# Performance work log

Measured on AMD Instinct MI355X. Metric: run time of the kernel, lower is better.

Reference implementation:

```python
import jax, jax.numpy as jnp
import numpy as np

D_X, D_H, N_I = 1024, 64, 16  # model dim, per-head dim (d_q=d_k=d_v), heads
BSZ, SEQ = 2, 2048


def _linear(x, W, b):
    return x @ W.T + b


def setup_inputs() -> dict:
    key = jax.random.key(0)
    ks = jax.random.split(key, 16)
    s_in = 1.0 / np.sqrt(D_X)
    s_hd = 1.0 / np.sqrt(N_I * D_H)
    return {
        "query": jax.random.normal(ks[0], (BSZ, SEQ, D_X), jnp.float32),
        "key": jax.random.normal(ks[1], (BSZ, SEQ, D_X), jnp.float32),
        "value": jax.random.normal(ks[2], (BSZ, SEQ, D_X), jnp.float32),
        "Wq": jax.random.normal(ks[3], (N_I * D_H, D_X), jnp.float32) * s_in,
        "bq": jnp.zeros((N_I * D_H,), jnp.float32),
        "Wk": jax.random.normal(ks[4], (N_I * D_H, D_X), jnp.float32) * s_in,
        "bk": jnp.zeros((N_I * D_H,), jnp.float32),
        "Wv": jax.random.normal(ks[5], (N_I * D_H, D_X), jnp.float32) * s_in,
        "bv": jnp.zeros((N_I * D_H,), jnp.float32),
        "Wxv": jax.random.normal(ks[6], (N_I * D_H, D_X), jnp.float32) * s_in,
        "bxv": jnp.zeros((N_I * D_H,), jnp.float32),
        "Wxo": jax.random.normal(ks[7], (D_X, N_I * D_H), jnp.float32) * s_hd,
        "bxo": jnp.zeros((D_X,), jnp.float32),
        "Wmo": jax.random.normal(ks[8], (D_X, N_I * D_H), jnp.float32) * s_hd,
        "bmo": jnp.zeros((D_X,), jnp.float32),
    }


def reference(query, key, value, Wq, bq, Wk, bk, Wv, bv, Wxv, bxv, Wxo, bxo, Wmo, bmo):
    bsz, seq, _ = query.shape

    def heads(x):  # (b, s, n_I*d) -> (b, h, s, d)
        return x.reshape(bsz, seq, N_I, D_H).transpose(0, 2, 1, 3)

    Q = heads(_linear(query, Wq, bq))
    K = heads(_linear(key, Wk, bk))
    V = heads(_linear(value, Wv, bv))

    dot = jnp.einsum('bhid,bhjd->bhij', Q, K) / jnp.sqrt(jnp.float32(D_H))
    attention = jax.nn.softmax(dot, axis=-1)  # dropout p=0 (eval)

    # use_xv=True: replace K with xV = W_xv(key) for the k_bar aggregation
    xV = heads(_linear(key, Wxv, bxv))

    k_bar = jnp.einsum('bhjd,bhij->bhid', xV, attention)
    v_bar = jnp.einsum('bhjd,bhij->bhid', V, attention)

    def merge(x):  # (b, h, s, d) -> (b, s, h*d)
        return x.transpose(0, 2, 1, 3).reshape(bsz, seq, N_I * D_H)

    x = _linear(merge(k_bar), Wxo, bxo)
    m = _linear(merge(v_bar), Wmo, bmo)
    return (x, m)
```

## Files before the change

kernel.cpp:

```cpp
#include <hip/hip_runtime.h>
#include <math.h>

typedef __bf16 bf16;
typedef __bf16 bf16x2 __attribute__((ext_vector_type(2)));
typedef __bf16 bf16x4 __attribute__((ext_vector_type(4)));
typedef __bf16 bf16x8 __attribute__((ext_vector_type(8)));
typedef float f32x4 __attribute__((ext_vector_type(4)));

#define SEQ 2048
#define DH 64
#define DX 1024
#define NH 16
#define LP 72

static __device__ __forceinline__ f32x4 mfma16(bf16x8 a, bf16x8 b, f32x4 c) {
    return __builtin_amdgcn_mfma_f32_16x16x32_bf16(a, b, c, 0, 0, 0);
}
static __device__ __forceinline__ bf16x8 cvt8(const float* __restrict__ p) {
    f32x4 a = *(const f32x4*)p;
    f32x4 b = *(const f32x4*)(p + 4);
    bf16x8 r;
    #pragma unroll
    for (int j = 0; j < 4; ++j) { r[j] = (bf16)a[j]; r[4 + j] = (bf16)b[j]; }
    return r;
}

#define GL16(gp, lp) __builtin_amdgcn_global_load_lds( \
    (const __attribute__((address_space(1))) void*)(gp), \
    (__attribute__((address_space(3))) void*)(lp), 16, 0, 0)


__global__ __launch_bounds__(256) void cvt_all(
    const float* __restrict__ q, const float* __restrict__ k,
    const float* __restrict__ v,
    const float* __restrict__ w0, const float* __restrict__ w1,
    const float* __restrict__ w2, const float* __restrict__ w3,
    const float* __restrict__ w4, const float* __restrict__ w5,
    bf16* __restrict__ out)
{
    const size_t i = (size_t)blockIdx.x * 2048 + threadIdx.x * 8;
    const int seg = (int)(i >> 20);
    const float* s;
    size_t off;
    if (seg < 4)       { s = q; off = i; }
    else if (seg < 8)  { s = k; off = i - (4ull << 20); }
    else if (seg < 12) { s = v; off = i - (8ull << 20); }
    else {
        const float* ww[6] = {w0, w1, w2, w3, w4, w5};
        s = ww[seg - 12]; off = i - ((size_t)seg << 20);
    }
    *(bf16x8*)(out + i) = cvt8(s + off);
}

struct G4 {
    const bf16* X[4]; const bf16* W[4]; const float* B[4];
    bf16* Yb[4]; float* Yf[4]; int xmode[4]; int ymode[4];
};

template<int BM>
__global__ __launch_bounds__(512) void gemm256(G4 a)
{
    constexpr int MREP = BM / 32;
    __shared__ __align__(16) bf16 As[2][BM * 64];
    __shared__ __align__(16) bf16 Bs[2][256 * 64];

    const int z = blockIdx.z;
    const bf16* __restrict__ X = a.X[z];
    const bf16* __restrict__ W = a.W[z];
    const int xmode = a.xmode[z], ymode = a.ymode[z];

    const int tid  = threadIdx.x;
    const int wid  = tid >> 6;
    const int lane = tid & 63;
    const int l16  = lane & 15;
    const int quad = lane >> 4;
    const int wm   = wid >> 2;
    const int wn   = wid & 3;
    const int m0 = blockIdx.y * BM;
    const int n0 = blockIdx.x * 256;

    const int srow8 = lane >> 3;
    const int sch   = (lane & 7) ^ srow8;

    f32x4 acc[MREP][4];
    #pragma unroll
    for (int i = 0; i < MREP; ++i)
        #pragma unroll
        for (int j = 0; j < 4; ++j) acc[i][j] = (f32x4){0.f,0.f,0.f,0.f};

    auto stage = [&](int buf, int kb) {
        #pragma unroll
        for (int g = 0; g < BM / 64; ++g) {
            const int row = g * 64 + wid * 8 + srow8;
            const bf16* src;
            if (xmode == 0) {
                src = X + (size_t)(m0 + row) * DX + kb * 64 + sch * 8;
            } else {
                const int m = m0 + row;
                const int b = m >> 11, s = m & 2047;
                src = X + ((size_t)(b * NH + kb) * SEQ + s) * DH + sch * 8;
            }
            GL16(src, &As[buf][(g * 64 + wid * 8) * 64]);
        }
        #pragma unroll
        for (int g = 0; g < 4; ++g) {
            const int row = g * 64 + wid * 8 + srow8;
            const bf16* src = W + (size_t)(n0 + row) * DX + kb * 64 + sch * 8;
            GL16(src, &Bs[buf][(g * 64 + wid * 8) * 64]);
        }
    };

    stage(0, 0);
    __syncthreads();

    int cur = 0;
    for (int kb = 0; kb < DX / 64; ++kb) {
        if (kb + 1 < DX / 64) stage(cur ^ 1, kb + 1);
        #pragma unroll
        for (int ks = 0; ks < 2; ++ks) {
            bf16x8 af[MREP], bfr[4];
            const int cc = (ks * 4 + quad) ^ (l16 & 7);
            #pragma unroll
            for (int mf = 0; mf < MREP; ++mf)
                af[mf] = *(const bf16x8*)&As[cur][(wm * (BM/2) + mf * 16 + l16) * 64 + cc * 8];
            #pragma unroll
            for (int nf = 0; nf < 4; ++nf)
                bfr[nf] = *(const bf16x8*)&Bs[cur][(wn * 64 + nf * 16 + l16) * 64 + cc * 8];
            #pragma unroll
            for (int mf = 0; mf < MREP; ++mf)
                #pragma unroll
                for (int nf = 0; nf < 4; ++nf)
                    acc[mf][nf] = mfma16(af[mf], bfr[nf], acc[mf][nf]);
        }
        __syncthreads();
        cur ^= 1;
    }

    #pragma unroll
    for (int nf = 0; nf < 4; ++nf) {
        const int col = n0 + wn * 64 + nf * 16 + l16;
        const float bvv = a.B[z][col];
        #pragma unroll
        for (int mf = 0; mf < MREP; ++mf) {
            #pragma unroll
            for (int r = 0; r < 4; ++r) {
                const int row = m0 + wm * (BM/2) + mf * 16 + quad * 4 + r;
                const float vv = acc[mf][nf][r] + bvv;
                if (ymode == 0) {
                    const int b = row >> 11, s = row & 2047;
                    const int h = col >> 6, d = col & 63;
                    a.Yb[z][((size_t)(b * NH + h) * SEQ + s) * DH + d] = (bf16)vv;
                } else {
                    a.Yf[z][(size_t)row * DX + col] = vv;
                }
            }
        }
    }
}

__global__ __launch_bounds__(256) void attn_fast(
    bf16* __restrict__ Q, const bf16* __restrict__ K,
    const bf16* __restrict__ V, const bf16* __restrict__ xV,
    bf16* __restrict__ VB)
{
    __shared__ __align__(16) bf16 Ks[2][64 * 64];
    __shared__ __align__(16) bf16 Vt [64 * LP];
    __shared__ __align__(16) bf16 xVt[64 * LP];
    __shared__ __align__(16) bf16 Pl[4][32 * LP];

    const int tid  = threadIdx.x;
    const int wave = tid >> 6;
    const int lane = tid & 63;
    const int l16  = lane & 15;
    const int quad = lane >> 4;
    const size_t hb = ((size_t)blockIdx.z * NH + blockIdx.y) * SEQ * DH;
    const int q0 = blockIdx.x * 128 + wave * 32;

    bf16x8 qf[2][2];
    #pragma unroll
    for (int mf = 0; mf < 2; ++mf)
        #pragma unroll
        for (int ks = 0; ks < 2; ++ks)
            qf[mf][ks] = *(const bf16x8*)(Q + hb + (size_t)(q0 + mf*16 + l16) * DH + ks*32 + quad*8);

    bf16x8 one8;
    #pragma unroll
    for (int j = 0; j < 8; ++j) one8[j] = (bf16)1.0f;

    f32x4 ov[2][4], oxv[2][4];
    f32x4 rsa[2];
    rsa[0] = (f32x4){0.f,0.f,0.f,0.f};
    rsa[1] = (f32x4){0.f,0.f,0.f,0.f};
    #pragma unroll
    for (int mf = 0; mf < 2; ++mf)
        #pragma unroll
        for (int c = 0; c < 4; ++c) {
            ov[mf][c]  = (f32x4){0.f,0.f,0.f,0.f};
            oxv[mf][c] = (f32x4){0.f,0.f,0.f,0.f};
        }

    const int krow = lane >> 3;
    const int kch  = (lane & 7) ^ krow;
    const int vkp = (tid & 31) * 2;
    const int vd0 = (tid >> 5) * 8;
    const float SCL = 0.125f * 1.4426950408889634f;

    bf16x8 pv0, pv1, px0, px1;
    {
        const bf16* kg = K + hb + (size_t)(wave*16 + krow) * DH + kch*8;
        GL16(kg,            &Ks[0][(wave*16 + 0) * 64]);
        GL16(kg + 8 * DH,   &Ks[0][(wave*16 + 8) * 64]);
        const size_t g0 = hb + (size_t)vkp * DH + vd0;
        pv0 = *(const bf16x8*)(V  + g0);
        pv1 = *(const bf16x8*)(V  + g0 + DH);
        px0 = *(const bf16x8*)(xV + g0);
        px1 = *(const bf16x8*)(xV + g0 + DH);
    }

    int c = 0;
    for (int kt = 0; kt < SEQ; kt += 64) {
        #pragma unroll
        for (int j = 0; j < 8; ++j) {
            *(bf16x2*)&Vt [(vd0 + j) * LP + vkp] = (bf16x2){pv0[j], pv1[j]};
            *(bf16x2*)&xVt[(vd0 + j) * LP + vkp] = (bf16x2){px0[j], px1[j]};
        }
        if (kt + 64 < SEQ) {
            const bf16* kg = K + hb + (size_t)(kt + 64 + wave*16 + krow) * DH + kch*8;
            GL16(kg,          &Ks[c ^ 1][(wave*16 + 0) * 64]);
            GL16(kg + 8 * DH, &Ks[c ^ 1][(wave*16 + 8) * 64]);
            const size_t g0 = hb + (size_t)(kt + 64 + vkp) * DH + vd0;
            pv0 = *(const bf16x8*)(V  + g0);
            pv1 = *(const bf16x8*)(V  + g0 + DH);
            px0 = *(const bf16x8*)(xV + g0);
            px1 = *(const bf16x8*)(xV + g0 + DH);
        }
        __asm__ volatile("s_waitcnt lgkmcnt(0)" ::: "memory");
        __builtin_amdgcn_s_barrier();
        __asm__ volatile("s_waitcnt vmcnt(6)" ::: "memory");
        __builtin_amdgcn_sched_barrier(0);

        f32x4 sf[4][2];
        #pragma unroll
        for (int mf = 0; mf < 4; ++mf)
            #pragma unroll
            for (int nf = 0; nf < 2; ++nf) sf[mf][nf] = (f32x4){0.f,0.f,0.f,0.f};
        __builtin_amdgcn_s_setprio(1);
        #pragma unroll
        for (int ks = 0; ks < 2; ++ks)
            #pragma unroll
            for (int mf = 0; mf < 4; ++mf) {
                bf16x8 kf = *(const bf16x8*)&Ks[c][(mf*16 + l16) * 64 +
                                                   (((ks*4 + quad) ^ (l16 & 7)) * 8)];
                sf[mf][0] = mfma16(kf, qf[0][ks], sf[mf][0]);
                sf[mf][1] = mfma16(kf, qf[1][ks], sf[mf][1]);
            }
        __builtin_amdgcn_s_setprio(0);

        #pragma unroll
        for (int nf = 0; nf < 2; ++nf)
            #pragma unroll
            for (int mf = 0; mf < 4; ++mf) {
                float p0 = __builtin_amdgcn_exp2f(sf[mf][nf][0] * SCL);
                float p1 = __builtin_amdgcn_exp2f(sf[mf][nf][1] * SCL);
                float p2 = __builtin_amdgcn_exp2f(sf[mf][nf][2] * SCL);
                float p3 = __builtin_amdgcn_exp2f(sf[mf][nf][3] * SCL);
                *(bf16x4*)&Pl[wave][(nf * 16 + l16) * LP + mf * 16 + quad * 4] =
                    (bf16x4){(bf16)p0, (bf16)p1, (bf16)p2, (bf16)p3};
            }
        __asm__ volatile("s_waitcnt lgkmcnt(0)" ::: "memory");
        __builtin_amdgcn_sched_barrier(0);

        __builtin_amdgcn_s_setprio(1);
        #pragma unroll
        for (int ks = 0; ks < 2; ++ks) {
            bf16x8 pa0 = *(const bf16x8*)&Pl[wave][(l16)      * LP + ks * 32 + quad * 8];
            bf16x8 pa1 = *(const bf16x8*)&Pl[wave][(16 + l16) * LP + ks * 32 + quad * 8];
            rsa[0] = mfma16(pa0, one8, rsa[0]);
            rsa[1] = mfma16(pa1, one8, rsa[1]);
            #pragma unroll
            for (int cc = 0; cc < 4; ++cc) {
                bf16x8 bv = *(const bf16x8*)&Vt [(cc * 16 + l16) * LP + ks * 32 + quad * 8];
                ov[0][cc]  = mfma16(pa0, bv, ov[0][cc]);
                ov[1][cc]  = mfma16(pa1, bv, ov[1][cc]);
                bf16x8 bx = *(const bf16x8*)&xVt[(cc * 16 + l16) * LP + ks * 32 + quad * 8];
                oxv[0][cc] = mfma16(pa0, bx, oxv[0][cc]);
                oxv[1][cc] = mfma16(pa1, bx, oxv[1][cc]);
            }
        }
        __builtin_amdgcn_s_setprio(0);

        __builtin_amdgcn_sched_barrier(0);
        __builtin_amdgcn_s_barrier();
        c ^= 1;
    }

    #pragma unroll
    for (int mf = 0; mf < 2; ++mf)
        #pragma unroll
        for (int r = 0; r < 4; ++r) {
            const int qrow = mf * 16 + quad * 4 + r;
            const float inv = 1.0f / rsa[mf][r];
            const size_t base = hb + (size_t)(q0 + qrow) * DH;
            #pragma unroll
            for (int cc = 0; cc < 4; ++cc) {
                const int d = cc * 16 + l16;
                Q [base + d] = (bf16)(oxv[mf][cc][r] * inv);
                VB[base + d] = (bf16)(ov[mf][cc][r]  * inv);
            }
        }
}


__global__ __launch_bounds__(256) void proj_gemm(
    const void* __restrict__ Xv, const float* __restrict__ W,
    const float* __restrict__ bias, void* __restrict__ Yv,
    int in_kind, int out_mode)
{
    __shared__ __align__(16) bf16 As[64 * LP];
    __shared__ __align__(16) bf16 Bs[128 * LP];
    const int tid  = threadIdx.x;
    const int wave = tid >> 6;
    const int lane = tid & 63;
    const int l16  = lane & 15;
    const int quad = lane >> 4;
    const int m0 = blockIdx.y * 64;
    const int n0 = blockIdx.x * 128;
    const int m_w = (wave >> 1) * 32;
    const int n_w = (wave & 1) * 64;
    const int ar = tid >> 2, ac = (tid & 3) * 16;
    const int br = tid >> 1, bc = (tid & 1) * 32;

    f32x4 acc[2][4];
    #pragma unroll
    for (int i = 0; i < 2; ++i)
        #pragma unroll
        for (int j = 0; j < 4; ++j) acc[i][j] = (f32x4){0.f,0.f,0.f,0.f};

    for (int kb = 0; kb < DX / 64; ++kb) {
        __syncthreads();
        if (in_kind == 0) {
            const float* xp = (const float*)Xv + (size_t)(m0 + ar) * DX + kb * 64 + ac;
            *(bf16x8*)&As[ar * LP + ac]     = cvt8(xp);
            *(bf16x8*)&As[ar * LP + ac + 8] = cvt8(xp + 8);
        } else {
            const bf16* xp = (const bf16*)Xv + ((size_t)kb * SEQ + (m0 + ar)) * DH + ac;
            *(bf16x8*)&As[ar * LP + ac]     = *(const bf16x8*)xp;
            *(bf16x8*)&As[ar * LP + ac + 8] = *(const bf16x8*)(xp + 8);
        }
        {
            const float* wp = W + (size_t)(n0 + br) * DX + kb * 64 + bc;
            #pragma unroll
            for (int g = 0; g < 4; ++g)
                *(bf16x8*)&Bs[br * LP + bc + g * 8] = cvt8(wp + g * 8);
        }
        __syncthreads();
        #pragma unroll
        for (int ks = 0; ks < 2; ++ks) {
            bf16x8 a0 = *(const bf16x8*)&As[(m_w + l16)      * LP + ks * 32 + quad * 8];
            bf16x8 a1 = *(const bf16x8*)&As[(m_w + 16 + l16) * LP + ks * 32 + quad * 8];
            #pragma unroll
            for (int nf = 0; nf < 4; ++nf) {
                bf16x8 b = *(const bf16x8*)&Bs[(n_w + nf * 16 + l16) * LP + ks * 32 + quad * 8];
                acc[0][nf] = mfma16(a0, b, acc[0][nf]);
                acc[1][nf] = mfma16(a1, b, acc[1][nf]);
            }
        }
    }
    #pragma unroll
    for (int mf = 0; mf < 2; ++mf)
        #pragma unroll
        for (int nf = 0; nf < 4; ++nf) {
            const int col = n0 + n_w + nf * 16 + l16;
            const float bvv = bias[col];
            #pragma unroll
            for (int r = 0; r < 4; ++r) {
                const int row = m0 + m_w + mf * 16 + quad * 4 + r;
                float v = acc[mf][nf][r] + bvv;
                if (out_mode == 0) {
                    int h = col >> 6, d = col & 63;
                    ((bf16*)Yv)[((size_t)h * SEQ + row) * DH + d] = (bf16)v;
                } else {
                    ((float*)Yv)[(size_t)row * DX + col] = v;
                }
            }
        }
}

__global__ __launch_bounds__(256) void attn_dual(
    bf16* __restrict__ Q, const bf16* __restrict__ K,
    const bf16* __restrict__ V, const bf16* __restrict__ xV,
    bf16* __restrict__ vb)
{
    __shared__ __align__(16) bf16 Ks [64 * LP];
    __shared__ __align__(16) bf16 Vt [64 * LP];
    __shared__ __align__(16) bf16 xVt[64 * LP];
    __shared__ __align__(16) bf16 Pl[4][32 * LP];
    const int tid  = threadIdx.x;
    const int h    = blockIdx.y;
    const int qt   = blockIdx.x;
    const int wave = tid >> 6;
    const int lane = tid & 63;
    const int l16  = lane & 15;
    const int quad = lane >> 4;
    const size_t hb = (size_t)h * SEQ * DH;
    const int q0 = qt * 128 + wave * 32;

    bf16x8 qf[2][2];
    #pragma unroll
    for (int mf = 0; mf < 2; ++mf)
        #pragma unroll
        for (int ks = 0; ks < 2; ++ks)
            qf[mf][ks] = *(const bf16x8*)(Q + hb + (size_t)(q0 + mf*16 + l16) * DH + ks*32 + quad*8);

    float mr[2][4], lr[2][4];
    f32x4 ov[2][4], oxv[2][4];
    #pragma unroll
    for (int mf = 0; mf < 2; ++mf)
        #pragma unroll
        for (int r = 0; r < 4; ++r) { mr[mf][r] = -1e30f; lr[mf][r] = 0.f; }
    #pragma unroll
    for (int mf = 0; mf < 2; ++mf)
        #pragma unroll
        for (int c = 0; c < 4; ++c) {
            ov[mf][c]  = (f32x4){0.f,0.f,0.f,0.f};
            oxv[mf][c] = (f32x4){0.f,0.f,0.f,0.f};
        }
    const int sr = tid >> 2, sc = (tid & 3) * 16;
    const int vkp = (tid & 31) * 2;
    const int vd0 = (tid >> 5) * 8;
    const float SCL = 0.125f * 1.4426950408889634f;

    for (int kt = 0; kt < SEQ; kt += 64) {
        __syncthreads();
        {
            const bf16* kpt = K + hb + (size_t)(kt + sr) * DH + sc;
            *(bf16x8*)&Ks[sr * LP + sc]     = *(const bf16x8*)kpt;
            *(bf16x8*)&Ks[sr * LP + sc + 8] = *(const bf16x8*)(kpt + 8);
            const size_t g0 = hb + (size_t)(kt + vkp) * DH + vd0;
            bf16x8 v0 = *(const bf16x8*)(V + g0);
            bf16x8 v1 = *(const bf16x8*)(V + g0 + DH);
            bf16x8 x0 = *(const bf16x8*)(xV + g0);
            bf16x8 x1 = *(const bf16x8*)(xV + g0 + DH);
            #pragma unroll
            for (int j = 0; j < 8; ++j) {
                *(bf16x2*)&Vt [(vd0 + j) * LP + vkp] = (bf16x2){v0[j], v1[j]};
                *(bf16x2*)&xVt[(vd0 + j) * LP + vkp] = (bf16x2){x0[j], x1[j]};
            }
        }
        __syncthreads();
        f32x4 sf[2][4];
        #pragma unroll
        for (int mf = 0; mf < 2; ++mf)
            #pragma unroll
            for (int nf = 0; nf < 4; ++nf) sf[mf][nf] = (f32x4){0.f,0.f,0.f,0.f};
        #pragma unroll
        for (int ks = 0; ks < 2; ++ks)
            #pragma unroll
            for (int nf = 0; nf < 4; ++nf) {
                bf16x8 bk = *(const bf16x8*)&Ks[(nf * 16 + l16) * LP + ks * 32 + quad * 8];
                sf[0][nf] = mfma16(qf[0][ks], bk, sf[0][nf]);
                sf[1][nf] = mfma16(qf[1][ks], bk, sf[1][nf]);
            }
        float mx[2][4], rs[2][4], alpha[2][4];
        #pragma unroll
        for (int mf = 0; mf < 2; ++mf)
            #pragma unroll
            for (int r = 0; r < 4; ++r) {
                float aa = fmaxf(sf[mf][0][r], sf[mf][1][r]);
                float bb = fmaxf(sf[mf][2][r], sf[mf][3][r]);
                mx[mf][r] = fmaxf(aa, bb) * SCL;
            }
        #pragma unroll
        for (int off = 1; off < 16; off <<= 1)
            #pragma unroll
            for (int mf = 0; mf < 2; ++mf)
                #pragma unroll
                for (int r = 0; r < 4; ++r)
                    mx[mf][r] = fmaxf(mx[mf][r], __shfl_xor(mx[mf][r], off, 64));
        #pragma unroll
        for (int mf = 0; mf < 2; ++mf)
            #pragma unroll
            for (int r = 0; r < 4; ++r) {
                float mnew = fmaxf(mr[mf][r], mx[mf][r]);
                alpha[mf][r] = exp2f(mr[mf][r] - mnew);
                mr[mf][r] = mnew;
            }
        bf16* pw = &Pl[wave][0];
        #pragma unroll
        for (int mf = 0; mf < 2; ++mf)
            #pragma unroll
            for (int r = 0; r < 4; ++r) rs[mf][r] = 0.f;
        #pragma unroll
        for (int mf = 0; mf < 2; ++mf)
            #pragma unroll
            for (int nf = 0; nf < 4; ++nf)
                #pragma unroll
                for (int r = 0; r < 4; ++r) {
                    float p = exp2f(sf[mf][nf][r] * SCL - mr[mf][r]);
                    rs[mf][r] += p;
                    pw[(mf * 16 + quad * 4 + r) * LP + nf * 16 + l16] = (bf16)p;
                }
        #pragma unroll
        for (int off = 1; off < 16; off <<= 1)
            #pragma unroll
            for (int mf = 0; mf < 2; ++mf)
                #pragma unroll
                for (int r = 0; r < 4; ++r)
                    rs[mf][r] += __shfl_xor(rs[mf][r], off, 64);
        #pragma unroll
        for (int mf = 0; mf < 2; ++mf)
            #pragma unroll
            for (int r = 0; r < 4; ++r)
                lr[mf][r] = lr[mf][r] * alpha[mf][r] + rs[mf][r];
        #pragma unroll
        for (int mf = 0; mf < 2; ++mf)
            #pragma unroll
            for (int c = 0; c < 4; ++c)
                #pragma unroll
                for (int r = 0; r < 4; ++r) {
                    ov[mf][c][r]  *= alpha[mf][r];
                    oxv[mf][c][r] *= alpha[mf][r];
                }
        __asm__ volatile("s_waitcnt lgkmcnt(0)" ::: "memory");
        #pragma unroll
        for (int ks = 0; ks < 2; ++ks) {
            bf16x8 pa0 = *(const bf16x8*)&Pl[wave][(l16)      * LP + ks * 32 + quad * 8];
            bf16x8 pa1 = *(const bf16x8*)&Pl[wave][(16 + l16) * LP + ks * 32 + quad * 8];
            #pragma unroll
            for (int c = 0; c < 4; ++c) {
                bf16x8 bv = *(const bf16x8*)&Vt [(c * 16 + l16) * LP + ks * 32 + quad * 8];
                ov[0][c]  = mfma16(pa0, bv, ov[0][c]);
                ov[1][c]  = mfma16(pa1, bv, ov[1][c]);
                bf16x8 bx = *(const bf16x8*)&xVt[(c * 16 + l16) * LP + ks * 32 + quad * 8];
                oxv[0][c] = mfma16(pa0, bx, oxv[0][c]);
                oxv[1][c] = mfma16(pa1, bx, oxv[1][c]);
            }
        }
    }
    #pragma unroll
    for (int mf = 0; mf < 2; ++mf)
        #pragma unroll
        for (int r = 0; r < 4; ++r) {
            const int s = q0 + mf * 16 + quad * 4 + r;
            const float inv = 1.0f / lr[mf][r];
            #pragma unroll
            for (int c = 0; c < 4; ++c) {
                const int d = c * 16 + l16;
                Q [hb + (size_t)s * DH + d] = (bf16)(oxv[mf][c][r] * inv);
                vb[hb + (size_t)s * DH + d] = (bf16)(ov[mf][c][r]  * inv);
            }
        }
}


extern "C" void kernel_launch(void* const* d_in, const int* in_sizes, int n_in,
                              void* d_out, int out_size, void* d_ws, size_t ws_size,
                              hipStream_t stream) {
    const float* query = (const float*)d_in[0];
    const float* key   = (const float*)d_in[1];
    const float* value = (const float*)d_in[2];
    const float* Wq  = (const float*)d_in[3];  const float* bq  = (const float*)d_in[4];
    const float* Wk  = (const float*)d_in[5];  const float* bk  = (const float*)d_in[6];
    const float* Wv  = (const float*)d_in[7];  const float* bv  = (const float*)d_in[8];
    const float* Wxv = (const float*)d_in[9];  const float* bxv = (const float*)d_in[10];
    const float* Wxo = (const float*)d_in[11]; const float* bxo = (const float*)d_in[12];
    const float* Wmo = (const float*)d_in[13]; const float* bmo = (const float*)d_in[14];

    float* out = (float*)d_out;
    const size_t SB = (size_t)SEQ * DX;
    const size_t M1 = 1ull << 20;

    dim3 blk(256);

    if (ws_size >= (76ull << 20)) {
        bf16* ws = (bf16*)d_ws;
        bf16* qb  = ws;
        bf16* kb  = ws + 4 * M1;
        bf16* vb  = ws + 8 * M1;
        bf16* Wqb = ws + 12 * M1;
        bf16* Wkb = Wqb + M1;
        bf16* Wvb = Wkb + M1;
        bf16* Wxvb= Wvb + M1;
        bf16* Wxob= Wxvb + M1;
        bf16* Wmob= Wxob + M1;
        bf16* Qs  = ws + 18 * M1;
        bf16* Kss = ws + 22 * M1;
        bf16* Vs  = ws + 26 * M1;
        bf16* xVs = ws + 30 * M1;
        bf16* VBs = ws + 34 * M1;

        cvt_all<<<9216, blk, 0, stream>>>(query, key, value,
                                          Wq, Wk, Wv, Wxv, Wxo, Wmo, ws + 0);

        G4 g1;
        g1.X[0]=qb;  g1.W[0]=Wqb;  g1.B[0]=bq;  g1.Yb[0]=Qs;  g1.Yf[0]=nullptr; g1.xmode[0]=0; g1.ymode[0]=0;
        g1.X[1]=kb;  g1.W[1]=Wkb;  g1.B[1]=bk;  g1.Yb[1]=Kss; g1.Yf[1]=nullptr; g1.xmode[1]=0; g1.ymode[1]=0;
        g1.X[2]=vb;  g1.W[2]=Wvb;  g1.B[2]=bv;  g1.Yb[2]=Vs;  g1.Yf[2]=nullptr; g1.xmode[2]=0; g1.ymode[2]=0;
        g1.X[3]=kb;  g1.W[3]=Wxvb; g1.B[3]=bxv; g1.Yb[3]=xVs; g1.Yf[3]=nullptr; g1.xmode[3]=0; g1.ymode[3]=0;
        gemm256<256><<<dim3(4, 16, 4), dim3(512), 0, stream>>>(g1);

        attn_fast<<<dim3(16, NH, 2), blk, 0, stream>>>(Qs, Kss, Vs, xVs, VBs);

        G4 g2;
        g2.X[0]=Qs;  g2.W[0]=Wxob; g2.B[0]=bxo; g2.Yb[0]=nullptr; g2.Yf[0]=out;          g2.xmode[0]=1; g2.ymode[0]=1;
        g2.X[1]=VBs; g2.W[1]=Wmob; g2.B[1]=bmo; g2.Yb[1]=nullptr; g2.Yf[1]=out + 2*SB;   g2.xmode[1]=1; g2.ymode[1]=1;
        g2.X[2]=Qs;  g2.W[2]=Wxob; g2.B[2]=bxo; g2.Yb[2]=nullptr; g2.Yf[2]=out;          g2.xmode[2]=1; g2.ymode[2]=1;
        g2.X[3]=Qs;  g2.W[3]=Wxob; g2.B[3]=bxo; g2.Yb[3]=nullptr; g2.Yf[3]=out;          g2.xmode[3]=1; g2.ymode[3]=1;
        gemm256<128><<<dim3(4, 32, 2), dim3(512), 0, stream>>>(g2);
    } else {
        bf16* Qs  = (bf16*)d_ws;
        bf16* Ksb = Qs  + SB;
        bf16* Vs  = Ksb + SB;
        bf16* xVs = Vs  + SB;
        bf16* vbs = xVs + SB;
        dim3 pg(8, 32);
        dim3 ag(16, NH);
        for (int b = 0; b < 2; ++b) {
            const float* q_b = query + (size_t)b * SB;
            const float* k_b = key   + (size_t)b * SB;
            const float* v_b = value + (size_t)b * SB;
            float* x_b = out + (size_t)b * SB;
            float* m_b = out + 2 * SB + (size_t)b * SB;
            proj_gemm<<<pg, blk, 0, stream>>>(q_b, Wq,  bq,  Qs,  0, 0);
            proj_gemm<<<pg, blk, 0, stream>>>(k_b, Wk,  bk,  Ksb, 0, 0);
            proj_gemm<<<pg, blk, 0, stream>>>(v_b, Wv,  bv,  Vs,  0, 0);
            proj_gemm<<<pg, blk, 0, stream>>>(k_b, Wxv, bxv, xVs, 0, 0);
            attn_dual<<<ag, blk, 0, stream>>>(Qs, Ksb, Vs, xVs, vbs);
            proj_gemm<<<pg, blk, 0, stream>>>(Qs,  Wxo, bxo, x_b, 1, 1);
            proj_gemm<<<pg, blk, 0, stream>>>(vbs, Wmo, bmo, m_b, 1, 1);
        }
    }
}
```

Baseline: 290.9 us.

## Pair attention waves to split V and xV outputs, remap GEMM block order

The attention kernel now runs 512 threads per block with waves working in pairs. Both waves of a pair compute the same 64-query scores, using half the rows each, and write P to shared memory. After a block barrier, one wave accumulates P·V and the other P·xV over all 64 rows, which halves the output accumulator registers per wave and makes each B-fragment load feed four MFMAs. The GEMM kernel also remaps block indices with a stride-8 swizzle to change tile scheduling order, likely for cache locality. The cost is an extra block-wide barrier per key tile, and every wave now computes the row-sum MFMAs for four fragments.

```diff
diff --git a/kernel.cpp b/kernel.cpp
--- a/kernel.cpp
+++ b/kernel.cpp
@@ -76,8 +76,13 @@
     const int quad = lane >> 4;
     const int wm   = wid >> 2;
     const int wn   = wid & 3;
-    const int m0 = blockIdx.y * BM;
-    const int n0 = blockIdx.x * 256;
+
+    const int nx = gridDim.x;
+    const int nt = nx * gridDim.y;
+    int t = blockIdx.x + nx * blockIdx.y;
+    t = (t & 7) * (nt >> 3) + (t >> 3);
+    const int n0 = (t % nx) * 256;
+    const int m0 = (t / nx) * BM;
 
     const int srow8 = lane >> 3;
     const int sch   = (lane & 7) ^ srow8;
@@ -158,7 +163,7 @@
     }
 }
 
-__global__ __launch_bounds__(256) void attn_fast(
+__global__ __launch_bounds__(512) void attn_pair(
     bf16* __restrict__ Q, const bf16* __restrict__ K,
     const bf16* __restrict__ V, const bf16* __restrict__ xV,
     bf16* __restrict__ VB)
@@ -166,77 +171,72 @@
     __shared__ __align__(16) bf16 Ks[2][64 * 64];
     __shared__ __align__(16) bf16 Vt [64 * LP];
     __shared__ __align__(16) bf16 xVt[64 * LP];
-    __shared__ __align__(16) bf16 Pl[4][32 * LP];
+    __shared__ __align__(16) bf16 Pl[4][64 * LP];
 
     const int tid  = threadIdx.x;
-    const int wave = tid >> 6;
+    const int wid  = tid >> 6;
     const int lane = tid & 63;
     const int l16  = lane & 15;
     const int quad = lane >> 4;
+    const int pair = wid >> 1;
+    const int half = wid & 1;
     const size_t hb = ((size_t)blockIdx.z * NH + blockIdx.y) * SEQ * DH;
-    const int q0 = blockIdx.x * 128 + wave * 32;
+    const int qp = blockIdx.x * 256 + pair * 64;
+    const int q0 = qp + half * 32;
 
     bf16x8 qf[2][2];
     #pragma unroll
-    for (int mf = 0; mf < 2; ++mf)
+    for (int nf = 0; nf < 2; ++nf)
         #pragma unroll
         for (int ks = 0; ks < 2; ++ks)
-            qf[mf][ks] = *(const bf16x8*)(Q + hb + (size_t)(q0 + mf*16 + l16) * DH + ks*32 + quad*8);
+            qf[nf][ks] = *(const bf16x8*)(Q + hb + (size_t)(q0 + nf*16 + l16) * DH + ks*32 + quad*8);
 
     bf16x8 one8;
     #pragma unroll
     for (int j = 0; j < 8; ++j) one8[j] = (bf16)1.0f;
 
-    f32x4 ov[2][4], oxv[2][4];
-    f32x4 rsa[2];
-    rsa[0] = (f32x4){0.f,0.f,0.f,0.f};
-    rsa[1] = (f32x4){0.f,0.f,0.f,0.f};
-    #pragma unroll
-    for (int mf = 0; mf < 2; ++mf)
-        #pragma unroll
-        for (int c = 0; c < 4; ++c) {
-            ov[mf][c]  = (f32x4){0.f,0.f,0.f,0.f};
-            oxv[mf][c] = (f32x4){0.f,0.f,0.f,0.f};
-        }
+    f32x4 ov[4][4];
+    f32x4 rsa[4];
+    #pragma unroll
+    for (int mf = 0; mf < 4; ++mf) {
+        rsa[mf] = (f32x4){0.f,0.f,0.f,0.f};
+        #pragma unroll
+        for (int c = 0; c < 4; ++c) ov[mf][c] = (f32x4){0.f,0.f,0.f,0.f};
+    }
 
     const int krow = lane >> 3;
     const int kch  = (lane & 7) ^ krow;
-    const int vkp = (tid & 31) * 2;
-    const int vd0 = (tid >> 5) * 8;
+    const bf16* __restrict__ vsrc = (tid & 256) ? xV : V;
+    bf16* __restrict__ vdst = (tid & 256) ? xVt : Vt;
+    const int t8  = tid & 255;
+    const int vkp = (t8 & 31) * 2;
+    const int vd0 = (t8 >> 5) * 8;
     const float SCL = 0.125f * 1.4426950408889634f;
 
-    bf16x8 pv0, pv1, px0, px1;
+    bf16x8 pv0, pv1;
     {
-        const bf16* kg = K + hb + (size_t)(wave*16 + krow) * DH + kch*8;
-        GL16(kg,            &Ks[0][(wave*16 + 0) * 64]);
-        GL16(kg + 8 * DH,   &Ks[0][(wave*16 + 8) * 64]);
+        const bf16* kg = K + hb + (size_t)(wid*8 + krow) * DH + kch*8;
+        GL16(kg, &Ks[0][(wid*8) * 64]);
         const size_t g0 = hb + (size_t)vkp * DH + vd0;
-        pv0 = *(const bf16x8*)(V  + g0);
-        pv1 = *(const bf16x8*)(V  + g0 + DH);
-        px0 = *(const bf16x8*)(xV + g0);
-        px1 = *(const bf16x8*)(xV + g0 + DH);
+        pv0 = *(const bf16x8*)(vsrc + g0);
+        pv1 = *(const bf16x8*)(vsrc + g0 + DH);
     }
 
     int c = 0;
     for (int kt = 0; kt < SEQ; kt += 64) {
         #pragma unroll
-        for (int j = 0; j < 8; ++j) {
-            *(bf16x2*)&Vt [(vd0 + j) * LP + vkp] = (bf16x2){pv0[j], pv1[j]};
-            *(bf16x2*)&xVt[(vd0 + j) * LP + vkp] = (bf16x2){px0[j], px1[j]};
-        }
+        for (int j = 0; j < 8; ++j)
+            *(bf16x2*)&vdst[(vd0 + j) * LP + vkp] = (bf16x2){pv0[j], pv1[j]};
         if (kt + 64 < SEQ) {
-            const bf16* kg = K + hb + (size_t)(kt + 64 + wave*16 + krow) * DH + kch*8;
-            GL16(kg,          &Ks[c ^ 1][(wave*16 + 0) * 64]);
-            GL16(kg + 8 * DH, &Ks[c ^ 1][(wave*16 + 8) * 64]);
+            const bf16* kg = K + hb + (size_t)(kt + 64 + wid*8 + krow) * DH + kch*8;
+            GL16(kg, &Ks[c ^ 1][(wid*8) * 64]);
             const size_t g0 = hb + (size_t)(kt + 64 + vkp) * DH + vd0;
-            pv0 = *(const bf16x8*)(V  + g0);
-            pv1 = *(const bf16x8*)(V  + g0 + DH);
-            px0 = *(const bf16x8*)(xV + g0);
-            px1 = *(const bf16x8*)(xV + g0 + DH);
+            pv0 = *(const bf16x8*)(vsrc + g0);
+            pv1 = *(const bf16x8*)(vsrc + g0 + DH);
         }
         __asm__ volatile("s_waitcnt lgkmcnt(0)" ::: "memory");
         __builtin_amdgcn_s_barrier();
-        __asm__ volatile("s_waitcnt vmcnt(6)" ::: "memory");
+        __asm__ volatile("s_waitcnt vmcnt(3)" ::: "memory");
         __builtin_amdgcn_sched_barrier(0);
 
         f32x4 sf[4][2];
@@ -264,27 +264,30 @@
                 float p1 = __builtin_amdgcn_exp2f(sf[mf][nf][1] * SCL);
                 float p2 = __builtin_amdgcn_exp2f(sf[mf][nf][2] * SCL);
                 float p3 = __builtin_amdgcn_exp2f(sf[mf][nf][3] * SCL);
-                *(bf16x4*)&Pl[wave][(nf * 16 + l16) * LP + mf * 16 + quad * 4] =
+                *(bf16x4*)&Pl[pair][(half*32 + nf*16 + l16) * LP + mf*16 + quad*4] =
                     (bf16x4){(bf16)p0, (bf16)p1, (bf16)p2, (bf16)p3};
             }
         __asm__ volatile("s_waitcnt lgkmcnt(0)" ::: "memory");
+        __builtin_amdgcn_s_barrier();
         __builtin_amdgcn_sched_barrier(0);
 
         __builtin_amdgcn_s_setprio(1);
         #pragma unroll
         for (int ks = 0; ks < 2; ++ks) {
-            bf16x8 pa0 = *(const bf16x8*)&Pl[wave][(l16)      * LP + ks * 32 + quad * 8];
-            bf16x8 pa1 = *(const bf16x8*)&Pl[wave][(16 + l16) * LP + ks * 32 + quad * 8];
-            rsa[0] = mfma16(pa0, one8, rsa[0]);
-            rsa[1] = mfma16(pa1, one8, rsa[1]);
+            bf16x8 pa[4];
+            #pragma unroll
+            for (int mf = 0; mf < 4; ++mf)
+                pa[mf] = *(const bf16x8*)&Pl[pair][(mf*16 + l16) * LP + ks*32 + quad*8];
+            #pragma unroll
+            for (int mf = 0; mf < 4; ++mf)
+                rsa[mf] = mfma16(pa[mf], one8, rsa[mf]);
+            const bf16* __restrict__ tile = half ? xVt : Vt;
             #pragma unroll
             for (int cc = 0; cc < 4; ++cc) {
-                bf16x8 bv = *(const bf16x8*)&Vt [(cc * 16 + l16) * LP + ks * 32 + quad * 8];
-                ov[0][cc]  = mfma16(pa0, bv, ov[0][cc]);
-                ov[1][cc]  = mfma16(pa1, bv, ov[1][cc]);
-                bf16x8 bx = *(const bf16x8*)&xVt[(cc * 16 + l16) * LP + ks * 32 + quad * 8];
-                oxv[0][cc] = mfma16(pa0, bx, oxv[0][cc]);
-                oxv[1][cc] = mfma16(pa1, bx, oxv[1][cc]);
+                bf16x8 bv = *(const bf16x8*)&tile[(cc*16 + l16) * LP + ks*32 + quad*8];
+                #pragma unroll
+                for (int mf = 0; mf < 4; ++mf)
+                    ov[mf][cc] = mfma16(pa[mf], bv, ov[mf][cc]);
             }
         }
         __builtin_amdgcn_s_setprio(0);
@@ -294,19 +297,17 @@
         c ^= 1;
     }
 
-    #pragma unroll
-    for (int mf = 0; mf < 2; ++mf)
+    bf16* __restrict__ outp = half ? Q : VB;
+    #pragma unroll
+    for (int mf = 0; mf < 4; ++mf)
         #pragma unroll
         for (int r = 0; r < 4; ++r) {
             const int qrow = mf * 16 + quad * 4 + r;
             const float inv = 1.0f / rsa[mf][r];
-            const size_t base = hb + (size_t)(q0 + qrow) * DH;
-            #pragma unroll
-            for (int cc = 0; cc < 4; ++cc) {
-                const int d = cc * 16 + l16;
-                Q [base + d] = (bf16)(oxv[mf][cc][r] * inv);
-                VB[base + d] = (bf16)(ov[mf][cc][r]  * inv);
-            }
+            const size_t base = hb + (size_t)(qp + qrow) * DH;
+            #pragma unroll
+            for (int cc = 0; cc < 4; ++cc)
+                outp[base + cc*16 + l16] = (bf16)(ov[mf][cc][r] * inv);
         }
 }
 
@@ -599,7 +600,7 @@
         g1.X[3]=kb;  g1.W[3]=Wxvb; g1.B[3]=bxv; g1.Yb[3]=xVs; g1.Yf[3]=nullptr; g1.xmode[3]=0; g1.ymode[3]=0;
         gemm256<256><<<dim3(4, 16, 4), dim3(512), 0, stream>>>(g1);
 
-        attn_fast<<<dim3(16, NH, 2), blk, 0, stream>>>(Qs, Kss, Vs, xVs, VBs);
+        attn_pair<<<dim3(8, NH, 2), dim3(512), 0, stream>>>(Qs, Kss, Vs, xVs, VBs);
 
         G4 g2;
         g2.X[0]=Qs;  g2.W[0]=Wxob; g2.B[0]=bxo; g2.Yb[0]=nullptr; g2.Yf[0]=out;          g2.xmode[0]=1; g2.ymode[0]=1;
```

Result: no change. 288.2 us (-0.9%).
